# Performance work log

Measured on AMD Instinct MI355X. Metric: run time of the kernel, lower is better.

## Reference

```python
import jax, jax.numpy as jnp
import numpy as np

B, C, H, W = 16, 256, 32, 32
K = 3          # kernel size
KK = K * K     # matrix_batch = 9 kernel positions
N = 256        # out_channels = n (power of 2, nstack = 1)


def setup_inputs() -> dict:
    key = jax.random.key(0)
    k1, k2, k3, k4 = jax.random.split(key, 4)
    s = 1.0 / np.sqrt(2.0)  # repo's 'regular' param init scale
    return {
        "x": jax.random.normal(k1, (B, C, H, W), jnp.float32),
        "twiddle1": jax.random.normal(k2, (KK, N - 1, 2, 2), jnp.float32) * s,
        "twiddle2": jax.random.normal(k3, (KK, N - 1, 2, 2), jnp.float32) * s,
        "bias": jax.random.normal(k4, (KK, N), jnp.float32) * 0.01,
    }


def _butterfly_tied(twiddle, x, increasing):
    """Tied-weight butterfly multiply.
    twiddle: (s, n-1, 2, 2); x: (b, s, n). At stride st, twiddle[:, st-1:2*st-1]
    (length st) is shared across the n/(2*st) blocks (matches butterfly_mult_torch).
    """
    b, s, n = x.shape
    m = n.bit_length() - 1  # log2(n)
    strides = [1 << i for i in range(m)]
    if not increasing:
        strides = strides[::-1]
    for st in strides:
        t = twiddle[:, st - 1:2 * st - 1]            # (s, st, 2, 2)
        xr = x.reshape(b, s, n // (2 * st), 2, st)   # (b, s, g, 2, st)
        # out[b,s,g,i,l] = sum_k t[s,l,i,k] * xr[b,s,g,k,l]
        x = jnp.einsum('slik,bsgkl->bsgil', t, xr).reshape(b, s, n)
    return x


def reference(x, twiddle1, twiddle2, bias):
    b, c, h, w = x.shape
    # im2col / F.unfold with kernel 3, pad 1, stride 1 -> (b, c, 9, h*w),
    # kernel positions in row-major order (matches torch unfold layout).
    xp = jnp.pad(x, ((0, 0), (0, 0), (1, 1), (1, 1)))
    patches = jnp.stack(
        [xp[:, :, i:i + h, j:j + w] for i in range(K) for j in range(K)], axis=2
    )  # (b, c, 9, h, w)
    inp = patches.reshape(b, c, KK, h * w).transpose(0, 3, 2, 1)
    inp = inp.reshape(b * h * w, KK, c)  # (batch*h*w, 9, c)
    # BB^T: B^T (decreasing stride) then B (increasing stride), bias on last.
    y = _butterfly_tied(twiddle1, inp, increasing=False)
    y = _butterfly_tied(twiddle2, y, increasing=True) + bias  # bias: (9, N)
    out = y.mean(axis=1)  # average over the 9 kernel positions -> (b*h*w, N)
    return out.reshape(b, h * w, N).transpose(0, 2, 1).reshape(b, N, h, w)
```

## Files before the change

### kernel.cpp

```cpp
#include <hip/hip_runtime.h>
#include <hip/hip_bf16.h>

typedef __attribute__((ext_vector_type(8))) short short8;
typedef __attribute__((ext_vector_type(4))) float float4v;

#define XT_ELEMS (16*34*34*256)
#define WG_ELEMS (9*4*2*8*128*8)
#define XT_BYTES (XT_ELEMS*2)
#define WG_BYTES (WG_ELEMS*2)

__global__ __launch_bounds__(256) void k_transpose(const float* __restrict__ x,
                                                   __hip_bfloat16* __restrict__ xT) {
  __shared__ float tile[256 * 33];
  int blk = blockIdx.x;
  int h = blk & 31, b = blk >> 5;
  int tid = threadIdx.x;
  {
    int w4 = (tid & 7) * 4, c0 = tid >> 3;
#pragma unroll
    for (int j = 0; j < 8; ++j) {
      int ci = c0 + 32 * j;
      float4 v = *(const float4*)&x[((b * 256 + ci) * 32 + h) * 32 + w4];
      *(float4*)&tile[ci * 33 + w4] = v;
    }
  }
  __syncthreads();
  {
    int c2 = (tid & 127) * 2, wbase = (tid >> 7) * 16;
#pragma unroll
    for (int i = 0; i < 16; ++i) {
      int w = wbase + i;
      __hip_bfloat162 pk;
      pk.x = __float2bfloat16(tile[c2 * 33 + w]);
      pk.y = __float2bfloat16(tile[(c2 + 1) * 33 + w]);
      *(__hip_bfloat162*)&xT[((b * 34 + h + 1) * 34 + (w + 1)) * 256 + c2] = pk;
    }
  }
  if (h < 2) {
    uint4 z4 = {0u, 0u, 0u, 0u};
    int edge = h * 33;
    uint4* rowp = (uint4*)&xT[((b * 34 + edge) * 34) * 256];
    for (int i = tid; i < 1088; i += 256) rowp[i] = z4;
    for (int i = tid; i < 1024; i += 256) {
      int hh = 1 + (i >> 5);
      int c16 = (i & 31) * 8;
      *(uint4*)&xT[((b * 34 + hh) * 34 + edge) * 256 + c16] = z4;
    }
  }
}

__global__ __launch_bounds__(256) void k_build_w(const float* __restrict__ tw1,
                                                 const float* __restrict__ tw2,
                                                 const float* __restrict__ bias,
                                                 __hip_bfloat16* __restrict__ Wg,
                                                 float* __restrict__ biasout) {
  __shared__ float mat[256 * 17];
  __shared__ __align__(16) float tws[2 * 255 * 4];
  int blk = blockIdx.x;
  int tid = threadIdx.x;
  if (blk == 144) {
    if (tid < 256) {
      float a = 0.f;
#pragma unroll
      for (int s = 0; s < 9; ++s) a += bias[s * 256 + tid];
      biasout[tid] = a * (1.f / 9.f);
    }
    return;
  }
  int sidx = blk >> 4;
  int colbase = (blk & 15) * 16;

  for (int i = tid; i < 255 * 4; i += 256) {
    tws[i]           = tw1[sidx * 255 * 4 + i];
    tws[255 * 4 + i] = tw2[sidx * 255 * 4 + i];
  }
  {
    int r = tid;
#pragma unroll
    for (int c = 0; c < 16; ++c) mat[r * 17 + c] = (r == colbase + c) ? 1.f : 0.f;
  }

  int c  = tid & 15;
  int pg = tid >> 4;
  for (int ph = 0; ph < 2; ++ph) {
    for (int si = 0; si < 8; ++si) {
      int lg = ph ? si : (7 - si);
      int st = 1 << lg;
      __syncthreads();
      float x0[8], x1[8], t0[8], t1[8], t2[8], t3[8];
#pragma unroll
      for (int i = 0; i < 8; ++i) {
        int qp = pg * 8 + i;
        int li = qp & (st - 1);
        int gi = qp >> lg;
        int p0 = (gi << (lg + 1)) | li;
        int p1 = p0 + st;
        float4 tv = *(const float4*)&tws[(ph * 255 + st - 1 + li) * 4];
        t0[i] = tv.x; t1[i] = tv.y; t2[i] = tv.z; t3[i] = tv.w;
        x0[i] = mat[p0 * 17 + c];
        x1[i] = mat[p1 * 17 + c];
      }
#pragma unroll
      for (int i = 0; i < 8; ++i) {
        int qp = pg * 8 + i;
        int li = qp & (st - 1);
        int gi = qp >> lg;
        int p0 = (gi << (lg + 1)) | li;
        int p1 = p0 + st;
        mat[p0 * 17 + c] = t0[i] * x0[i] + t1[i] * x1[i];
        mat[p1 * 17 + c] = t2[i] * x0[i] + t3[i] * x1[i];
      }
    }
  }
  __syncthreads();

  for (int idx = tid; idx < 256 * 16; idx += 256) {
    int r = idx >> 4, cc = idx & 15;
    int cg = colbase + cc;
    int pr = cg >> 6, qq = (cg >> 3) & 7, c8 = cg & 7;
    int nt = r >> 7, nl = r & 127;
    int o = ((((sidx * 4 + pr) * 2 + nt) * 8 + qq) * 128 + nl) * 8 + c8;
    Wg[o] = __float2bfloat16(mat[r * 17 + cc] * (1.f / 9.f));
  }
}

#define LDS_A_SZ 16384
#define LDS_B_SZ (8 * 136 * 16)

__global__ __launch_bounds__(512, 4) void k_gemm(const __hip_bfloat16* __restrict__ xT,
                                                 const __hip_bfloat16* __restrict__ Wg,
                                                 const float* __restrict__ biasout,
                                                 float* __restrict__ out) {
  __shared__ __align__(16) char lds[2 * LDS_A_SZ + LDS_B_SZ];
  const char* WgB = (const char*)Wg;
  const char* xTB = (const char*)xT;

  int blk = blockIdx.x;
  int nt = blk & 1;
  int pt = (blk >> 1) & 15;
  int b  = blk >> 5;
  int h0 = pt * 2;

  int tid  = threadIdx.x;
  int lane = tid & 63;
  int wave = tid >> 6;
  int wk = wave >> 2;
  int wm = (wave >> 1) & 1;
  int wn = wave & 1;
  int q0 = lane >> 4;
  int q  = q0 + wk * 4;
  int l16 = lane & 15;

  float4v acc[4][2];
#pragma unroll
  for (int r = 0; r < 4; ++r)
#pragma unroll
    for (int j = 0; j < 2; ++j) acc[r][j] = (float4v){0.f, 0.f, 0.f, 0.f};

  int aoff[4];
#pragma unroll
  for (int r = 0; r < 4; ++r) aoff[r] = (q * 128 + wm * 64 + r * 16 + l16) * 16;
  int boff[2];
#pragma unroll
  for (int j = 0; j < 2; ++j) {
    int p = wn * 32 + j * 16 + l16;
    boff[j] = 2 * LDS_A_SZ + (q * 136 + (p >> 5) * 34 + (p & 31)) * 16;
  }

  auto stage_a = [&](int step, int buf) {
    int p = step / 9, s = step - p * 9;
    const char* g = WgB + (((s * 4 + p) * 2 + nt) * 16384);
#pragma unroll
    for (int i = 0; i < 2; ++i) {
      int slotbase = i * 512 + wave * 64;
      __builtin_amdgcn_global_load_lds(
          (const __attribute__((address_space(1))) void*)(g + (slotbase + lane) * 16),
          (__attribute__((address_space(3))) void*)(lds + buf * LDS_A_SZ + slotbase * 16),
          16, 0, 0);
    }
  };

  auto stage_b = [&](int p) {
#pragma unroll
    for (int i = 0; i < 3; ++i) {
      int slot = i * 512 + tid;
      if (slot < 1088) {
        int qq  = slot / 136;
        int pos = slot - qq * 136;
        int hh  = pos / 34;
        int ww  = pos - hh * 34;
        const char* g = xTB + (((b * 34 + h0 + hh) * 34 + ww) * 256 +
                               p * 64 + qq * 8) * 2;
        __builtin_amdgcn_global_load_lds(
            (const __attribute__((address_space(1))) void*)g,
            (__attribute__((address_space(3))) void*)(lds + 2 * LDS_A_SZ +
                                                     (i * 512 + wave * 64) * 16),
            16, 0, 0);
      }
    }
  };

  auto do_step = [&](int step) {
    int p = step / 9, s = step - p * 9;
    int si = s / 3, sj = s - si * 3;
    int soff = (si * 34 + sj) * 16;
    int abase = (step & 1) * LDS_A_SZ;
    short8 af[4], bfr[2];
#pragma unroll
    for (int r = 0; r < 4; ++r) af[r] = *(const short8*)(lds + abase + aoff[r]);
#pragma unroll
    for (int j = 0; j < 2; ++j) bfr[j] = *(const short8*)(lds + boff[j] + soff);
#pragma unroll
    for (int r = 0; r < 4; ++r)
#pragma unroll
      for (int j = 0; j < 2; ++j)
        acc[r][j] = __builtin_amdgcn_mfma_f32_16x16x32_bf16(af[r], bfr[j], acc[r][j], 0, 0, 0);
  };

  stage_a(0, 0);
  stage_b(0);
  __syncthreads();
  for (int step = 0; step < 36; ++step) {
    int p = step / 9, s = step - p * 9;
    if (s == 8) {
      if (p < 3) stage_a(step + 1, (step + 1) & 1);
      do_step(step);
      __syncthreads();
      if (p < 3) { stage_b(p + 1); __syncthreads(); }
    } else {
      stage_a(step + 1, (step + 1) & 1);
      do_step(step);
      __syncthreads();
    }
  }

  {
    int pr = wm * 2 + wn;
    __syncthreads();
    if (wk == 1) {
#pragma unroll
      for (int r = 0; r < 4; ++r)
        *(float4v*)(lds + ((pr * 4 + r) * 64 + lane) * 16) = acc[r][0];
    }
    __syncthreads();
    if (wk == 0) {
#pragma unroll
      for (int r = 0; r < 4; ++r)
        acc[r][0] += *(const float4v*)(lds + ((pr * 4 + r) * 64 + lane) * 16);
    }
    __syncthreads();
    if (wk == 0) {
#pragma unroll
      for (int r = 0; r < 4; ++r)
        *(float4v*)(lds + ((pr * 4 + r) * 64 + lane) * 16) = acc[r][1];
    }
    __syncthreads();
    if (wk == 1) {
#pragma unroll
      for (int r = 0; r < 4; ++r)
        acc[r][1] += *(const float4v*)(lds + ((pr * 4 + r) * 64 + lane) * 16);
    }
  }

  int nbase = nt * 128 + wm * 64;
  if (wk == 0) {
    int pp = wn * 32 + l16;
    int hr = h0 + (pp >> 5), wc = pp & 31;
#pragma unroll
    for (int r = 0; r < 4; ++r) {
      float4v v = acc[r][0];
#pragma unroll
      for (int reg = 0; reg < 4; ++reg) {
        int n = nbase + r * 16 + q0 * 4 + reg;
        out[((b * 256 + n) * 32 + hr) * 32 + wc] = v[reg] + biasout[n];
      }
    }
  } else {
    int pp = wn * 32 + 16 + l16;
    int hr = h0 + (pp >> 5), wc = pp & 31;
#pragma unroll
    for (int r = 0; r < 4; ++r) {
      float4v v = acc[r][1];
#pragma unroll
      for (int reg = 0; reg < 4; ++reg) {
        int n = nbase + r * 16 + q0 * 4 + reg;
        out[((b * 256 + n) * 32 + hr) * 32 + wc] = v[reg] + biasout[n];
      }
    }
  }
}

extern "C" void kernel_launch(void* const* d_in, const int* in_sizes, int n_in,
                              void* d_out, int out_size, void* d_ws, size_t ws_size,
                              hipStream_t stream) {
  const float* x    = (const float*)d_in[0];
  const float* tw1  = (const float*)d_in[1];
  const float* tw2  = (const float*)d_in[2];
  const float* bias = (const float*)d_in[3];
  float* out = (float*)d_out;

  char* ws = (char*)d_ws;
  __hip_bfloat16* xT = (__hip_bfloat16*)ws;
  __hip_bfloat16* Wg = (__hip_bfloat16*)(ws + XT_BYTES);
  float* biasout     = (float*)(ws + XT_BYTES + WG_BYTES);

  k_transpose<<<512, 256, 0, stream>>>(x, xT);
  k_build_w<<<145, 256, 0, stream>>>(tw1, tw2, bias, Wg, biasout);
  k_gemm<<<512, 512, 0, stream>>>(xT, Wg, biasout, out);
}
```

Before: 118.8 us.

## Switch GEMM to 32x32x16 MFMA with 4-wave blocks and larger per-wave tiles

Rewrites the GEMM kernel to use 32x32x16 bf16 MFMA instructions instead of 16x16x32. Blocks shrink from 8 waves to 4, so each wave now covers a 64x64 output tile with a two-way K split across wave pairs, and the staging loops are rewritten to match. The aim is fewer LDS fragment reads per MFMA and better operand reuse. In exchange each block has less parallelism to hide latency, accumulator register pressure is higher, and the cross-wave reduction now moves 16-wide vectors.

```diff
diff --git a/kernel.cpp b/kernel.cpp
--- a/kernel.cpp
+++ b/kernel.cpp
@@ -3,6 +3,7 @@
 
 typedef __attribute__((ext_vector_type(8))) short short8;
 typedef __attribute__((ext_vector_type(4))) float float4v;
+typedef __attribute__((ext_vector_type(16))) float float16v;
 
 #define XT_ELEMS (16*34*34*256)
 #define WG_ELEMS (9*4*2*8*128*8)
@@ -124,14 +125,15 @@
   }
 }
 
-#define LDS_A_SZ 16384
+#define ABUF 16384
+#define BBASE (2 * ABUF)
 #define LDS_B_SZ (8 * 136 * 16)
 
-__global__ __launch_bounds__(512, 4) void k_gemm(const __hip_bfloat16* __restrict__ xT,
+__global__ __launch_bounds__(256, 2) void k_gemm(const __hip_bfloat16* __restrict__ xT,
                                                  const __hip_bfloat16* __restrict__ Wg,
                                                  const float* __restrict__ biasout,
                                                  float* __restrict__ out) {
-  __shared__ __align__(16) char lds[2 * LDS_A_SZ + LDS_B_SZ];
+  __shared__ __align__(64) char lds[2 * ABUF + LDS_B_SZ];
   const char* WgB = (const char*)Wg;
   const char* xTB = (const char*)xT;
 
@@ -144,57 +146,59 @@
   int tid  = threadIdx.x;
   int lane = tid & 63;
   int wave = tid >> 6;
-  int wk = wave >> 2;
-  int wm = (wave >> 1) & 1;
-  int wn = wave & 1;
-  int q0 = lane >> 4;
-  int q  = q0 + wk * 4;
-  int l16 = lane & 15;
-
-  float4v acc[4][2];
-#pragma unroll
-  for (int r = 0; r < 4; ++r)
-#pragma unroll
-    for (int j = 0; j < 2; ++j) acc[r][j] = (float4v){0.f, 0.f, 0.f, 0.f};
-
-  int aoff[4];
-#pragma unroll
-  for (int r = 0; r < 4; ++r) aoff[r] = (q * 128 + wm * 64 + r * 16 + l16) * 16;
-  int boff[2];
-#pragma unroll
-  for (int j = 0; j < 2; ++j) {
-    int p = wn * 32 + j * 16 + l16;
-    boff[j] = 2 * LDS_A_SZ + (q * 136 + (p >> 5) * 34 + (p & 31)) * 16;
-  }
+  int wm = wave & 1;
+  int wk = wave >> 1;
+  int half = lane >> 5;
+  int l31 = lane & 31;
+
+  float16v acc[2][2];
+#pragma unroll
+  for (int mt = 0; mt < 2; ++mt)
+#pragma unroll
+    for (int p2 = 0; p2 < 2; ++p2)
+#pragma unroll
+      for (int e = 0; e < 16; ++e) acc[mt][p2][e] = 0.f;
+
+  int aoff[2][2], boff[2][2];
+#pragma unroll
+  for (int mt = 0; mt < 2; ++mt)
+#pragma unroll
+    for (int ks = 0; ks < 2; ++ks)
+      aoff[mt][ks] = ((wk * 4 + ks * 2 + half) * 128 + wm * 64 + mt * 32 + l31) * 16;
+#pragma unroll
+  for (int p2 = 0; p2 < 2; ++p2)
+#pragma unroll
+    for (int ks = 0; ks < 2; ++ks)
+      boff[p2][ks] = BBASE + ((wk * 4 + ks * 2 + half) * 136 + p2 * 34 + l31) * 16;
 
   auto stage_a = [&](int step, int buf) {
     int p = step / 9, s = step - p * 9;
     const char* g = WgB + (((s * 4 + p) * 2 + nt) * 16384);
 #pragma unroll
-    for (int i = 0; i < 2; ++i) {
-      int slotbase = i * 512 + wave * 64;
+    for (int i = 0; i < 4; ++i) {
+      int slotbase = i * 256 + wave * 64;
       __builtin_amdgcn_global_load_lds(
           (const __attribute__((address_space(1))) void*)(g + (slotbase + lane) * 16),
-          (__attribute__((address_space(3))) void*)(lds + buf * LDS_A_SZ + slotbase * 16),
+          (__attribute__((address_space(3))) void*)(lds + buf * ABUF + slotbase * 16),
           16, 0, 0);
     }
   };
 
   auto stage_b = [&](int p) {
 #pragma unroll
-    for (int i = 0; i < 3; ++i) {
-      int slot = i * 512 + tid;
+    for (int i = 0; i < 5; ++i) {
+      int slot = i * 256 + tid;
       if (slot < 1088) {
-        int qq  = slot / 136;
-        int pos = slot - qq * 136;
+        int gq  = slot / 136;
+        int pos = slot - gq * 136;
         int hh  = pos / 34;
         int ww  = pos - hh * 34;
         const char* g = xTB + (((b * 34 + h0 + hh) * 34 + ww) * 256 +
-                               p * 64 + qq * 8) * 2;
+                               p * 64 + gq * 8) * 2;
         __builtin_amdgcn_global_load_lds(
             (const __attribute__((address_space(1))) void*)g,
-            (__attribute__((address_space(3))) void*)(lds + 2 * LDS_A_SZ +
-                                                     (i * 512 + wave * 64) * 16),
+            (__attribute__((address_space(3))) void*)(lds + BBASE +
+                                                     (i * 256 + wave * 64) * 16),
             16, 0, 0);
       }
     }
@@ -204,17 +208,24 @@
     int p = step / 9, s = step - p * 9;
     int si = s / 3, sj = s - si * 3;
     int soff = (si * 34 + sj) * 16;
-    int abase = (step & 1) * LDS_A_SZ;
-    short8 af[4], bfr[2];
-#pragma unroll
-    for (int r = 0; r < 4; ++r) af[r] = *(const short8*)(lds + abase + aoff[r]);
-#pragma unroll
-    for (int j = 0; j < 2; ++j) bfr[j] = *(const short8*)(lds + boff[j] + soff);
-#pragma unroll
-    for (int r = 0; r < 4; ++r)
-#pragma unroll
-      for (int j = 0; j < 2; ++j)
-        acc[r][j] = __builtin_amdgcn_mfma_f32_16x16x32_bf16(af[r], bfr[j], acc[r][j], 0, 0, 0);
+    int abase = (step & 1) * ABUF;
+    short8 af[2][2], bf[2][2];
+#pragma unroll
+    for (int mt = 0; mt < 2; ++mt)
+#pragma unroll
+      for (int ks = 0; ks < 2; ++ks) af[mt][ks] = *(const short8*)(lds + abase + aoff[mt][ks]);
+#pragma unroll
+    for (int p2 = 0; p2 < 2; ++p2)
+#pragma unroll
+      for (int ks = 0; ks < 2; ++ks) bf[p2][ks] = *(const short8*)(lds + boff[p2][ks] + soff);
+#pragma unroll
+    for (int ks = 0; ks < 2; ++ks)
+#pragma unroll
+      for (int mt = 0; mt < 2; ++mt)
+#pragma unroll
+        for (int p2 = 0; p2 < 2; ++p2)
+          acc[mt][p2] = __builtin_amdgcn_mfma_f32_32x32x16_bf16(af[mt][ks], bf[p2][ks],
+                                                                acc[mt][p2], 0, 0, 0);
   };
 
   stage_a(0, 0);
@@ -235,56 +246,67 @@
   }
 
   {
-    int pr = wm * 2 + wn;
     __syncthreads();
     if (wk == 1) {
 #pragma unroll
-      for (int r = 0; r < 4; ++r)
-        *(float4v*)(lds + ((pr * 4 + r) * 64 + lane) * 16) = acc[r][0];
+      for (int p2 = 0; p2 < 2; ++p2)
+        *(float16v*)(lds + ((wm * 2 + p2) * 64 + lane) * 64) = acc[0][p2];
     }
     __syncthreads();
     if (wk == 0) {
 #pragma unroll
-      for (int r = 0; r < 4; ++r)
-        acc[r][0] += *(const float4v*)(lds + ((pr * 4 + r) * 64 + lane) * 16);
+      for (int p2 = 0; p2 < 2; ++p2)
+        acc[0][p2] += *(const float16v*)(lds + ((wm * 2 + p2) * 64 + lane) * 64);
     }
     __syncthreads();
     if (wk == 0) {
 #pragma unroll
-      for (int r = 0; r < 4; ++r)
-        *(float4v*)(lds + ((pr * 4 + r) * 64 + lane) * 16) = acc[r][1];
+      for (int p2 = 0; p2 < 2; ++p2)
+        *(float16v*)(lds + ((wm * 2 + p2) * 64 + lane) * 64) = acc[1][p2];
     }
     __syncthreads();
     if (wk == 1) {
 #pragma unroll
-      for (int r = 0; r < 4; ++r)
-        acc[r][1] += *(const float4v*)(lds + ((pr * 4 + r) * 64 + lane) * 16);
-    }
-  }
-
-  int nbase = nt * 128 + wm * 64;
+      for (int p2 = 0; p2 < 2; ++p2)
+        acc[1][p2] += *(const float16v*)(lds + ((wm * 2 + p2) * 64 + lane) * 64);
+    }
+  }
+
+  int wc = l31;
   if (wk == 0) {
-    int pp = wn * 32 + l16;
-    int hr = h0 + (pp >> 5), wc = pp & 31;
-#pragma unroll
-    for (int r = 0; r < 4; ++r) {
-      float4v v = acc[r][0];
-#pragma unroll
-      for (int reg = 0; reg < 4; ++reg) {
-        int n = nbase + r * 16 + q0 * 4 + reg;
-        out[((b * 256 + n) * 32 + hr) * 32 + wc] = v[reg] + biasout[n];
+    float bv[16];
+#pragma unroll
+    for (int reg = 0; reg < 16; ++reg) {
+      int row = (reg & 3) + 8 * (reg >> 2) + 4 * half;
+      bv[reg] = biasout[nt * 128 + wm * 64 + row];
+    }
+#pragma unroll
+    for (int p2 = 0; p2 < 2; ++p2) {
+      int hr = h0 + p2;
+      float16v v = acc[0][p2];
+#pragma unroll
+      for (int reg = 0; reg < 16; ++reg) {
+        int row = (reg & 3) + 8 * (reg >> 2) + 4 * half;
+        int n = nt * 128 + wm * 64 + row;
+        out[((b * 256 + n) * 32 + hr) * 32 + wc] = v[reg] + bv[reg];
       }
     }
   } else {
-    int pp = wn * 32 + 16 + l16;
-    int hr = h0 + (pp >> 5), wc = pp & 31;
-#pragma unroll
-    for (int r = 0; r < 4; ++r) {
-      float4v v = acc[r][1];
-#pragma unroll
-      for (int reg = 0; reg < 4; ++reg) {
-        int n = nbase + r * 16 + q0 * 4 + reg;
-        out[((b * 256 + n) * 32 + hr) * 32 + wc] = v[reg] + biasout[n];
+    float bv[16];
+#pragma unroll
+    for (int reg = 0; reg < 16; ++reg) {
+      int row = (reg & 3) + 8 * (reg >> 2) + 4 * half;
+      bv[reg] = biasout[nt * 128 + wm * 64 + 32 + row];
+    }
+#pragma unroll
+    for (int p2 = 0; p2 < 2; ++p2) {
+      int hr = h0 + p2;
+      float16v v = acc[1][p2];
+#pragma unroll
+      for (int reg = 0; reg < 16; ++reg) {
+        int row = (reg & 3) + 8 * (reg >> 2) + 4 * half;
+        int n = nt * 128 + wm * 64 + 32 + row;
+        out[((b * 256 + n) * 32 + hr) * 32 + wc] = v[reg] + bv[reg];
       }
     }
   }
@@ -306,5 +328,5 @@
 
   k_transpose<<<512, 256, 0, stream>>>(x, xT);
   k_build_w<<<145, 256, 0, stream>>>(tw1, tw2, bias, Wg, biasout);
-  k_gemm<<<512, 512, 0, stream>>>(xT, Wg, biasout, out);
+  k_gemm<<<512, 256, 0, stream>>>(xT, Wg, biasout, out);
 }
```

New measurement: 122.7 us. 3.2% more time.
